# Kernel tuning notes

Measured on AMD Instinct MI355X. Metric: run time of the kernel, lower is better.

The kernel has to match this reference:

```python
import jax, jax.numpy as jnp
import numpy as np

B, P, D = 256, 4, 768   # batch, num_meta_paths, embedding_dim*3
U = 32                  # user_count
IN = P * D              # Linear in_features


def setup_inputs() -> dict:
    key = jax.random.key(0)
    k1, k2, k3 = jax.random.split(key, 3)
    weight = jax.random.normal(k1, (B, P, D), dtype=jnp.float32)
    # Stacked per-user Linear params (torch nn.Linear: y = x @ W.T + b).
    # We store W_spec as [U, IN, D] so y_u = x @ W_spec[u] + b_spec[u].
    scale = 1.0 / np.sqrt(IN)
    W_spec = jax.random.uniform(k2, (U, IN, D), dtype=jnp.float32, minval=-scale, maxval=scale)
    b_spec = jax.random.uniform(k3, (U, D), dtype=jnp.float32, minval=-scale, maxval=scale)
    return {"weight": weight, "W_spec": W_spec, "b_spec": b_spec}


def reference(weight, W_spec, b_spec):
    # weight: [B, P, D]
    prompt_emb = weight.reshape(weight.shape[0], -1)                 # [B, P*D]
    # Fused batched GEMM over users (replaces the loop of U Linear calls + cat):
    task_specific = jnp.einsum('bi,uio->ubo', prompt_emb, W_spec) + b_spec[:, None, :]  # [U, B, D]
    task_specific = task_specific.reshape(U * weight.shape[0], D)    # cat along dim 0, user-major
    mean_emb = jnp.mean(weight, axis=1)                              # [B, D]
    return (task_specific, mean_emb)
```

## Files before the change

kernel.cpp:

```cpp
#include <hip/hip_runtime.h>
#include <hip/hip_bf16.h>


#define U_CNT  32
#define BROWS  256
#define DDIM   768
#define KDIM   3072
#define BK     32
#define BN     64
#define NT     12
#define KITERS 96
#define WSTRIDE 40

typedef float  f32x4 __attribute__((ext_vector_type(4)));
typedef __bf16 bf16x8 __attribute__((ext_vector_type(8)));

__global__ __launch_bounds__(256, 3) void coldprompt_gemm(
    const float* __restrict__ A,
    const float* __restrict__ Wsp,
    const float* __restrict__ bsp,
    float* __restrict__ out)
{
    __shared__ __align__(16) __bf16 wT[2][BN * WSTRIDE];

    const int tid  = threadIdx.x;
    const int lane = tid & 63;
    const int wave = tid >> 6;
    const int bid  = blockIdx.x;
    const int u    = bid / NT;
    const int n0   = (bid % NT) * BN;

    const float* __restrict__ Wu = Wsp + (size_t)u * (KDIM * DDIM);

    const int sd = tid & 63;
    const int sk = (tid >> 6) * 8;

    const int fcol = lane & 15;
    const int fk8  = (lane >> 4) * 8;

    f32x4 acc[4][4];
#pragma unroll
    for (int i = 0; i < 4; ++i)
#pragma unroll
        for (int j = 0; j < 4; ++j)
            acc[i][j] = (f32x4){0.f, 0.f, 0.f, 0.f};

    {
        const float* src = Wu + (size_t)sk * DDIM + n0 + sd;
        bf16x8 wv;
#pragma unroll
        for (int j = 0; j < 8; ++j) wv[j] = (__bf16)src[(size_t)j * DDIM];
        *(bf16x8*)&wT[0][sd * WSTRIDE + sk] = wv;
    }

    const float* __restrict__ arow = A + (size_t)(wave * 64 + fcol) * KDIM + fk8;

    int cur = 0;
    for (int kb = 0; kb < KITERS; ++kb) {
        __syncthreads();

        float wreg[8];
        if (kb + 1 < KITERS) {
            const float* src = Wu + (size_t)((kb + 1) * BK + sk) * DDIM + n0 + sd;
#pragma unroll
            for (int j = 0; j < 8; ++j) wreg[j] = src[(size_t)j * DDIM];
        }

        bf16x8 afrag[4];
#pragma unroll
        for (int mf = 0; mf < 4; ++mf) {
            const float* ap = arow + (size_t)(mf * 16) * KDIM + kb * BK;
            f32x4 a0 = *(const f32x4*)ap;
            f32x4 a1 = *(const f32x4*)(ap + 4);
#pragma unroll
            for (int j = 0; j < 4; ++j) {
                afrag[mf][j]     = (__bf16)a0[j];
                afrag[mf][4 + j] = (__bf16)a1[j];
            }
        }

        bf16x8 wfrag[4];
#pragma unroll
        for (int nf = 0; nf < 4; ++nf)
            wfrag[nf] = *(bf16x8*)&wT[cur][(nf * 16 + fcol) * WSTRIDE + fk8];

#pragma unroll
        for (int mf = 0; mf < 4; ++mf)
#pragma unroll
            for (int nf = 0; nf < 4; ++nf)
                acc[mf][nf] = __builtin_amdgcn_mfma_f32_16x16x32_bf16(
                    afrag[mf], wfrag[nf], acc[mf][nf], 0, 0, 0);

        if (kb + 1 < KITERS) {
            bf16x8 wv;
#pragma unroll
            for (int j = 0; j < 8; ++j) wv[j] = (__bf16)wreg[j];
            *(bf16x8*)&wT[cur ^ 1][sd * WSTRIDE + sk] = wv;
        }
        cur ^= 1;
    }

#pragma unroll
    for (int nf = 0; nf < 4; ++nf) {
        const int col  = n0 + nf * 16 + fcol;
        const float bias = bsp[u * DDIM + col];
#pragma unroll
        for (int mf = 0; mf < 4; ++mf) {
            const int rowb = wave * 64 + mf * 16 + ((lane >> 4) * 4);
            float* op = out + (size_t)(u * BROWS + rowb) * DDIM + col;
#pragma unroll
            for (int j = 0; j < 4; ++j)
                op[(size_t)j * DDIM] = acc[mf][nf][j] + bias;
        }
    }
}

__global__ void coldprompt_mean(const float* __restrict__ w, float* __restrict__ out) {
    const int b = blockIdx.x;
    const int d = threadIdx.x * 4;
    const float* p = w + (size_t)b * (4 * DDIM) + d;
    f32x4 s0 = *(const f32x4*)p;
    f32x4 s1 = *(const f32x4*)(p + DDIM);
    f32x4 s2 = *(const f32x4*)(p + 2 * DDIM);
    f32x4 s3 = *(const f32x4*)(p + 3 * DDIM);
    f32x4 m = (s0 + s1 + s2 + s3) * 0.25f;
    *(f32x4*)(out + (size_t)b * DDIM + d) = m;
}

extern "C" void kernel_launch(void* const* d_in, const int* in_sizes, int n_in,
                              void* d_out, int out_size, void* d_ws, size_t ws_size,
                              hipStream_t stream) {
    const float* weight = (const float*)d_in[0];
    const float* Wsp    = (const float*)d_in[1];
    const float* bsp    = (const float*)d_in[2];
    float* out = (float*)d_out;

    coldprompt_gemm<<<U_CNT * NT, 256, 0, stream>>>(weight, Wsp, bsp, out);

    float* mean_out = out + (size_t)U_CNT * BROWS * DDIM;
    coldprompt_mean<<<BROWS, 192, 0, stream>>>(weight, mean_out);
}
```

Baseline: 533.8 us.

## Split GEMM rows across two blocks, remap blocks for XCD locality, deepen W prefetch

The batch dimension is split into two 128-row tiles, doubling the grid from 384 to 768 blocks so the 256 CUs get more work and latency hiding. Block IDs are remapped so that the two M-tiles sharing a W column slice land on the same XCD (bid&7), which lets W be reused from L2. The W staging now keeps two register sets and prefetches two K-steps ahead inside a 2x unrolled loop. The cost is that each W slice is converted and staged into LDS twice, once per M-tile, and each block issues half as many MFMAs per LDS read.

```diff
diff --git a/kernel.cpp b/kernel.cpp
--- a/kernel.cpp
+++ b/kernel.cpp
@@ -7,6 +7,8 @@
 #define DDIM   768
 #define KDIM   3072
 #define BK     32
+#define BM     128
+#define MT     2
 #define BN     64
 #define NT     12
 #define KITERS 96
@@ -26,11 +28,18 @@
     const int tid  = threadIdx.x;
     const int lane = tid & 63;
     const int wave = tid >> 6;
-    const int bid  = blockIdx.x;
-    const int u    = bid / NT;
-    const int n0   = (bid % NT) * BN;
 
-    const float* __restrict__ Wu = Wsp + (size_t)u * (KDIM * DDIM);
+    const int bid = blockIdx.x;
+    const int x   = bid & 7;
+    const int jj  = bid >> 3;
+    const int i   = ((jj >> 1) << 3) + x;
+    const int mt  = jj & 1;
+    const int u   = i / NT;
+    const int nt  = i - u * NT;
+    const int n0  = nt * BN;
+    const int m0  = mt * BM;
+
+    const float* __restrict__ Wu = Wsp + (size_t)u * (KDIM * DDIM) + n0;
 
     const int sd = tid & 63;
     const int sk = (tid >> 6) * 8;
@@ -38,79 +47,76 @@
     const int fcol = lane & 15;
     const int fk8  = (lane >> 4) * 8;
 
-    f32x4 acc[4][4];
+    f32x4 acc[2][4];
 #pragma unroll
-    for (int i = 0; i < 4; ++i)
+    for (int a = 0; a < 2; ++a)
 #pragma unroll
-        for (int j = 0; j < 4; ++j)
-            acc[i][j] = (f32x4){0.f, 0.f, 0.f, 0.f};
+        for (int b = 0; b < 4; ++b)
+            acc[a][b] = (f32x4){0.f, 0.f, 0.f, 0.f};
 
-    {
-        const float* src = Wu + (size_t)sk * DDIM + n0 + sd;
-        bf16x8 wv;
-#pragma unroll
-        for (int j = 0; j < 8; ++j) wv[j] = (__bf16)src[(size_t)j * DDIM];
-        *(bf16x8*)&wT[0][sd * WSTRIDE + sk] = wv;
+    float rgA[8], rgB[8];
+
+#define STAGE(kb, rg) do {                                                  \
+    const float* s_ = Wu + (size_t)((kb) * BK + sk) * DDIM + sd;            \
+    _Pragma("unroll") for (int q = 0; q < 8; ++q)                           \
+        rg[q] = s_[(size_t)q * DDIM];                                       \
+} while (0)
+
+#define WWRITE(rg, buf) do {                                                \
+    bf16x8 wv_;                                                             \
+    _Pragma("unroll") for (int q = 0; q < 8; ++q) wv_[q] = (__bf16)rg[q];   \
+    *(bf16x8*)&wT[buf][sd * WSTRIDE + sk] = wv_;                            \
+} while (0)
+
+    STAGE(0, rgA);
+    STAGE(1, rgB);
+    WWRITE(rgA, 0);
+    STAGE(2, rgA);
+
+    const float* __restrict__ arow = A + (size_t)(m0 + wave * 32 + fcol) * KDIM + fk8;
+
+#define ITER(kb, RD, buf) do {                                              \
+    __syncthreads();                                                        \
+    bf16x8 af_[2];                                                          \
+    _Pragma("unroll") for (int mf = 0; mf < 2; ++mf) {                      \
+        const float* ap = arow + (size_t)(mf * 16) * KDIM + (kb) * BK;      \
+        f32x4 a0 = *(const f32x4*)ap;                                       \
+        f32x4 a1 = *(const f32x4*)(ap + 4);                                 \
+        _Pragma("unroll") for (int q = 0; q < 4; ++q) {                     \
+            af_[mf][q]     = (__bf16)a0[q];                                 \
+            af_[mf][4 + q] = (__bf16)a1[q];                                 \
+        }                                                                   \
+    }                                                                       \
+    bf16x8 wf_[4];                                                          \
+    _Pragma("unroll") for (int nf = 0; nf < 4; ++nf)                        \
+        wf_[nf] = *(bf16x8*)&wT[buf][(nf * 16 + fcol) * WSTRIDE + fk8];     \
+    _Pragma("unroll") for (int mf = 0; mf < 2; ++mf)                        \
+        _Pragma("unroll") for (int nf = 0; nf < 4; ++nf)                    \
+            acc[mf][nf] = __builtin_amdgcn_mfma_f32_16x16x32_bf16(          \
+                af_[mf], wf_[nf], acc[mf][nf], 0, 0, 0);                    \
+    if ((kb) + 1 < KITERS) WWRITE(RD, (buf) ^ 1);                           \
+    if ((kb) + 3 < KITERS) STAGE((kb) + 3, RD);                             \
+} while (0)
+
+    for (int kb = 0; kb < KITERS; kb += 2) {
+        ITER(kb,     rgB, 0);
+        ITER(kb + 1, rgA, 1);
     }
-
-    const float* __restrict__ arow = A + (size_t)(wave * 64 + fcol) * KDIM + fk8;
-
-    int cur = 0;
-    for (int kb = 0; kb < KITERS; ++kb) {
-        __syncthreads();
-
-        float wreg[8];
-        if (kb + 1 < KITERS) {
-            const float* src = Wu + (size_t)((kb + 1) * BK + sk) * DDIM + n0 + sd;
-#pragma unroll
-            for (int j = 0; j < 8; ++j) wreg[j] = src[(size_t)j * DDIM];
-        }
-
-        bf16x8 afrag[4];
-#pragma unroll
-        for (int mf = 0; mf < 4; ++mf) {
-            const float* ap = arow + (size_t)(mf * 16) * KDIM + kb * BK;
-            f32x4 a0 = *(const f32x4*)ap;
-            f32x4 a1 = *(const f32x4*)(ap + 4);
-#pragma unroll
-            for (int j = 0; j < 4; ++j) {
-                afrag[mf][j]     = (__bf16)a0[j];
-                afrag[mf][4 + j] = (__bf16)a1[j];
-            }
-        }
-
-        bf16x8 wfrag[4];
-#pragma unroll
-        for (int nf = 0; nf < 4; ++nf)
-            wfrag[nf] = *(bf16x8*)&wT[cur][(nf * 16 + fcol) * WSTRIDE + fk8];
-
-#pragma unroll
-        for (int mf = 0; mf < 4; ++mf)
-#pragma unroll
-            for (int nf = 0; nf < 4; ++nf)
-                acc[mf][nf] = __builtin_amdgcn_mfma_f32_16x16x32_bf16(
-                    afrag[mf], wfrag[nf], acc[mf][nf], 0, 0, 0);
-
-        if (kb + 1 < KITERS) {
-            bf16x8 wv;
-#pragma unroll
-            for (int j = 0; j < 8; ++j) wv[j] = (__bf16)wreg[j];
-            *(bf16x8*)&wT[cur ^ 1][sd * WSTRIDE + sk] = wv;
-        }
-        cur ^= 1;
-    }
+#undef ITER
+#undef STAGE
+#undef WWRITE
 
 #pragma unroll
     for (int nf = 0; nf < 4; ++nf) {
         const int col  = n0 + nf * 16 + fcol;
         const float bias = bsp[u * DDIM + col];
 #pragma unroll
-        for (int mf = 0; mf < 4; ++mf) {
-            const int rowb = wave * 64 + mf * 16 + ((lane >> 4) * 4);
+        for (int mf = 0; mf < 2; ++mf) {
+            const int rowb = m0 + wave * 32 + mf * 16 + ((lane >> 4) * 4);
             float* op = out + (size_t)(u * BROWS + rowb) * DDIM + col;
 #pragma unroll
-            for (int j = 0; j < 4; ++j)
-                op[(size_t)j * DDIM] = acc[mf][nf][j] + bias;
+            for (int q = 0; q < 4; ++q)
+                op[(size_t)q * DDIM] = acc[mf][nf][q] + bias;
         }
     }
 }
@@ -135,7 +141,7 @@
     const float* bsp    = (const float*)d_in[2];
     float* out = (float*)d_out;
 
-    coldprompt_gemm<<<U_CNT * NT, 256, 0, stream>>>(weight, Wsp, bsp, out);
+    coldprompt_gemm<<<U_CNT * NT * MT, 256, 0, stream>>>(weight, Wsp, bsp, out);
 
     float* mean_out = out + (size_t)U_CNT * BROWS * DDIM;
     coldprompt_mean<<<BROWS, 192, 0, stream>>>(weight, mean_out);
```

Result: no change. 526.1 us (-1.5%).
